# Optimization experiments

Measured on AMD Instinct MI355X. Metric: run time of the kernel, lower is better.

Reference implementation:

```python
import jax, jax.numpy as jnp
import numpy as np

CHANNELS = 512
SE_CHANNELS = 32


def setup_inputs() -> dict:
    key = jax.random.key(0)
    k_x, k_w1, k_b1, k_w2, k_b2 = jax.random.split(key, 5)
    c, se = CHANNELS, SE_CHANNELS
    x = jax.random.normal(k_x, (256, c, 32, 32), dtype=jnp.float32)
    # torch.nn.Linear default init: U(-1/sqrt(fan_in), 1/sqrt(fan_in))
    s1 = 1.0 / np.sqrt(c)
    s2 = 1.0 / np.sqrt(se)
    fc1_w = jax.random.uniform(k_w1, (se, c), jnp.float32, -s1, s1)
    fc1_b = jax.random.uniform(k_b1, (se,), jnp.float32, -s1, s1)
    fc2_w = jax.random.uniform(k_w2, (2 * c, se), jnp.float32, -s2, s2)
    fc2_b = jax.random.uniform(k_b2, (2 * c,), jnp.float32, -s2, s2)
    return {"x": x, "fc1_w": fc1_w, "fc1_b": fc1_b, "fc2_w": fc2_w, "fc2_b": fc2_b}


def reference(x, fc1_w, fc1_b, fc2_w, fc2_b):
    b, c, h, w = x.shape
    # squeeze: global average pool -> [B, C]
    y = jnp.mean(x, axis=(2, 3))
    # excitation MLP
    y = jax.nn.relu(y @ fc1_w.T + fc1_b)          # [B, se]
    y = y @ fc2_w.T + fc2_b                        # [B, 2C]
    scale, bias = y[:, :c], y[:, c:]
    scale = jax.nn.sigmoid(scale)[:, :, None, None]  # [B, C, 1, 1]
    bias = bias[:, :, None, None]
    return x * scale + bias
```

## Files before the change

kernel.cpp:

```cpp
#include <hip/hip_runtime.h>
#include <math.h>

#define BATCH 256
#define CH 512
#define SE_CH 32
#define HW 1024
#define CHUNK_B 64
#define NCHUNK (BATCH / CHUNK_B)
#define CHUNK_PLANES (CHUNK_B * CH)

typedef float f32x4 __attribute__((ext_vector_type(4)));

__global__ void se_mean_kernel(const float* __restrict__ x,
                               float* __restrict__ mean,
                               int nplanes) {
    const int lane = threadIdx.x & 63;
    const int wave_in_block = threadIdx.x >> 6;
    const int waves_per_block = blockDim.x >> 6;
    int wid = blockIdx.x * waves_per_block + wave_in_block;
    const int nwaves = gridDim.x * waves_per_block;

    for (int p = wid; p < nplanes; p += nwaves) {
        const f32x4* px = (const f32x4*)(x + (size_t)p * HW);
        float s = 0.0f;
#pragma unroll
        for (int j = 0; j < 4; ++j) {
            f32x4 v = px[lane + j * 64];
            s += (v.x + v.y) + (v.z + v.w);
        }
#pragma unroll
        for (int off = 32; off > 0; off >>= 1)
            s += __shfl_down(s, off, 64);
        if (lane == 0)
            mean[p] = s * (1.0f / (float)HW);
    }
}

__global__ void se_fc_kernel(const float* __restrict__ mean,
                             const float* __restrict__ fc1_w,
                             const float* __restrict__ fc1_b,
                             const float* __restrict__ fc2_w,
                             const float* __restrict__ fc2_b,
                             float* __restrict__ scale,
                             float* __restrict__ bias) {
    const int b = blockIdx.x;
    const int t = threadIdx.x;
    __shared__ float m[CH];
    __shared__ float se[SE_CH];

    for (int i = t; i < CH; i += blockDim.x)
        m[i] = mean[b * CH + i];
    __syncthreads();

    {
        const int o = t >> 3;
        const int p = t & 7;
        float acc = 0.0f;
        const float* wr = fc1_w + o * CH + p * 64;
        const float* mr = m + p * 64;
#pragma unroll 16
        for (int k = 0; k < 64; ++k)
            acc = fmaf(wr[k], mr[k], acc);
#pragma unroll
        for (int off = 4; off > 0; off >>= 1)
            acc += __shfl_xor(acc, off, 8);
        if (p == 0)
            se[o] = fmaxf(acc + fc1_b[o], 0.0f);
    }
    __syncthreads();

    for (int o = t; o < 2 * CH; o += blockDim.x) {
        float acc = fc2_b[o];
        const float* wr = fc2_w + o * SE_CH;
#pragma unroll
        for (int k = 0; k < SE_CH; ++k)
            acc = fmaf(wr[k], se[k], acc);
        if (o < CH)
            scale[b * CH + o] = 1.0f / (1.0f + expf(-acc));
        else
            bias[b * CH + (o - CH)] = acc;
    }
}

__global__ void se_apply_kernel(const float* __restrict__ x,
                                const float* __restrict__ scale,
                                const float* __restrict__ bias,
                                float* __restrict__ out,
                                size_t n4) {
    size_t i = blockIdx.x * (size_t)blockDim.x + threadIdx.x;
    const size_t stride = (size_t)gridDim.x * blockDim.x;
    const f32x4* x4 = (const f32x4*)x;
    f32x4* o4 = (f32x4*)out;

    for (; i < n4; i += stride) {
        const int plane = (int)(i >> 8);
        const float s = scale[plane];
        const float bi = bias[plane];
        f32x4 v = x4[i];
        f32x4 r;
        r.x = fmaf(v.x, s, bi);
        r.y = fmaf(v.y, s, bi);
        r.z = fmaf(v.z, s, bi);
        r.w = fmaf(v.w, s, bi);
        __builtin_nontemporal_store(r, &o4[i]);
    }
}

extern "C" void kernel_launch(void* const* d_in, const int* in_sizes, int n_in,
                              void* d_out, int out_size, void* d_ws, size_t ws_size,
                              hipStream_t stream) {
    const float* x     = (const float*)d_in[0];
    const float* fc1_w = (const float*)d_in[1];
    const float* fc1_b = (const float*)d_in[2];
    const float* fc2_w = (const float*)d_in[3];
    const float* fc2_b = (const float*)d_in[4];
    float* out = (float*)d_out;

    const int nplanes = BATCH * CH;
    float* mean  = (float*)d_ws;
    float* scale = mean + nplanes;
    float* bias  = scale + nplanes;

    for (int ck = 0; ck < NCHUNK; ++ck) {
        const size_t po = (size_t)ck * CHUNK_PLANES;
        const float* xc = x + po * HW;
        float* oc = out + po * HW;

        se_mean_kernel<<<1024, 256, 0, stream>>>(xc, mean + po, CHUNK_PLANES);

        se_fc_kernel<<<CHUNK_B, 256, 0, stream>>>(mean + po, fc1_w, fc1_b,
                                                  fc2_w, fc2_b,
                                                  scale + po, bias + po);

        se_apply_kernel<<<2048, 256, 0, stream>>>(xc, scale + po, bias + po, oc,
                                                  (size_t)CHUNK_PLANES * (HW / 4));
    }
}
```

Baseline: 303.6 us.

## Fuse FC into apply blocks and overlap next chunk's mean with current apply

Replaces the three kernels per chunk with one fused kernel. Apply blocks recompute the small FC MLP locally for their 64-channel slice, and extra blocks compute the channel means of the next chunk in the same launch. This software-pipelines the mean pass against the apply pass, so the mean read of chunk k+1 can hit cache while chunk k is written. It also removes the separate FC launch. In exchange, fc1 is computed redundantly 8 times per batch element, and the mean and apply blocks compete for bandwidth inside each launch.

```diff
diff --git a/kernel.cpp b/kernel.cpp
--- a/kernel.cpp
+++ b/kernel.cpp
@@ -8,101 +8,104 @@
 #define CHUNK_B 64
 #define NCHUNK (BATCH / CHUNK_B)
 #define CHUNK_PLANES (CHUNK_B * CH)
+#define SUBS 8
+#define CPS (CH / SUBS)
+#define NA_BLOCKS (CHUNK_B * SUBS)
+#define NM_BLOCKS 512
 
 typedef float f32x4 __attribute__((ext_vector_type(4)));
 
-__global__ void se_mean_kernel(const float* __restrict__ x,
-                               float* __restrict__ mean,
-                               int nplanes) {
-    const int lane = threadIdx.x & 63;
-    const int wave_in_block = threadIdx.x >> 6;
-    const int waves_per_block = blockDim.x >> 6;
-    int wid = blockIdx.x * waves_per_block + wave_in_block;
-    const int nwaves = gridDim.x * waves_per_block;
-
-    for (int p = wid; p < nplanes; p += nwaves) {
-        const f32x4* px = (const f32x4*)(x + (size_t)p * HW);
-        float s = 0.0f;
-#pragma unroll
-        for (int j = 0; j < 4; ++j) {
-            f32x4 v = px[lane + j * 64];
-            s += (v.x + v.y) + (v.z + v.w);
-        }
-#pragma unroll
-        for (int off = 32; off > 0; off >>= 1)
-            s += __shfl_down(s, off, 64);
-        if (lane == 0)
-            mean[p] = s * (1.0f / (float)HW);
-    }
-}
-
-__global__ void se_fc_kernel(const float* __restrict__ mean,
-                             const float* __restrict__ fc1_w,
-                             const float* __restrict__ fc1_b,
-                             const float* __restrict__ fc2_w,
-                             const float* __restrict__ fc2_b,
-                             float* __restrict__ scale,
-                             float* __restrict__ bias) {
-    const int b = blockIdx.x;
+__global__ __launch_bounds__(256) void se_fused(
+        const float* __restrict__ x,
+        float* __restrict__ out,
+        float* __restrict__ mean_ws,
+        const float* __restrict__ fc1_w,
+        const float* __restrict__ fc1_b,
+        const float* __restrict__ fc2_w,
+        const float* __restrict__ fc2_b,
+        int na, int apply_b0, int mean_p0, int mean_np) {
     const int t = threadIdx.x;
     __shared__ float m[CH];
     __shared__ float se[SE_CH];
+    __shared__ float sc[CPS];
+    __shared__ float bi[CPS];
 
-    for (int i = t; i < CH; i += blockDim.x)
-        m[i] = mean[b * CH + i];
-    __syncthreads();
+    if ((int)blockIdx.x < na) {
+        const int ab = blockIdx.x;
+        const int b = apply_b0 + (ab >> 3);
+        const int sub = ab & 7;
 
-    {
-        const int o = t >> 3;
-        const int p = t & 7;
-        float acc = 0.0f;
-        const float* wr = fc1_w + o * CH + p * 64;
-        const float* mr = m + p * 64;
-#pragma unroll 16
-        for (int k = 0; k < 64; ++k)
-            acc = fmaf(wr[k], mr[k], acc);
+        for (int i = t; i < CH; i += 256)
+            m[i] = mean_ws[(size_t)b * CH + i];
+        __syncthreads();
+
+        {
+            const int o = t >> 3;
+            const int p = t & 7;
+            const float* wr = fc1_w + o * CH;
+            float acc = 0.0f;
 #pragma unroll
-        for (int off = 4; off > 0; off >>= 1)
-            acc += __shfl_xor(acc, off, 8);
-        if (p == 0)
-            se[o] = fmaxf(acc + fc1_b[o], 0.0f);
-    }
-    __syncthreads();
+            for (int j = 0; j < 64; ++j) {
+                const int k = p + 8 * j;
+                acc = fmaf(wr[k], m[k], acc);
+            }
+            acc += __shfl_xor(acc, 4, 8);
+            acc += __shfl_xor(acc, 2, 8);
+            acc += __shfl_xor(acc, 1, 8);
+            if (p == 0)
+                se[o] = fmaxf(acc + fc1_b[o], 0.0f);
+        }
+        __syncthreads();
 
-    for (int o = t; o < 2 * CH; o += blockDim.x) {
-        float acc = fc2_b[o];
-        const float* wr = fc2_w + o * SE_CH;
+        if (t < 2 * CPS) {
+            const int c = sub * CPS + (t & (CPS - 1));
+            const int o = (t < CPS) ? c : (CH + c);
+            float acc = fc2_b[o];
+            const float* wr = fc2_w + o * SE_CH;
 #pragma unroll
-        for (int k = 0; k < SE_CH; ++k)
-            acc = fmaf(wr[k], se[k], acc);
-        if (o < CH)
-            scale[b * CH + o] = 1.0f / (1.0f + expf(-acc));
-        else
-            bias[b * CH + (o - CH)] = acc;
-    }
-}
+            for (int k = 0; k < SE_CH; ++k)
+                acc = fmaf(wr[k], se[k], acc);
+            if (t < CPS)
+                sc[t] = 1.0f / (1.0f + expf(-acc));
+            else
+                bi[t - CPS] = acc;
+        }
+        __syncthreads();
 
-__global__ void se_apply_kernel(const float* __restrict__ x,
-                                const float* __restrict__ scale,
-                                const float* __restrict__ bias,
-                                float* __restrict__ out,
-                                size_t n4) {
-    size_t i = blockIdx.x * (size_t)blockDim.x + threadIdx.x;
-    const size_t stride = (size_t)gridDim.x * blockDim.x;
-    const f32x4* x4 = (const f32x4*)x;
-    f32x4* o4 = (f32x4*)out;
-
-    for (; i < n4; i += stride) {
-        const int plane = (int)(i >> 8);
-        const float s = scale[plane];
-        const float bi = bias[plane];
-        f32x4 v = x4[i];
-        f32x4 r;
-        r.x = fmaf(v.x, s, bi);
-        r.y = fmaf(v.y, s, bi);
-        r.z = fmaf(v.z, s, bi);
-        r.w = fmaf(v.w, s, bi);
-        __builtin_nontemporal_store(r, &o4[i]);
+        const size_t base = ((size_t)b * CH + (size_t)sub * CPS) * HW;
+        const f32x4* xp = (const f32x4*)(x + base);
+        f32x4* op = (f32x4*)(out + base);
+#pragma unroll 4
+        for (int p = 0; p < CPS; ++p) {
+            const float s = sc[p];
+            const float bb = bi[p];
+            f32x4 v = xp[p * 256 + t];
+            f32x4 r;
+            r.x = fmaf(v.x, s, bb);
+            r.y = fmaf(v.y, s, bb);
+            r.z = fmaf(v.z, s, bb);
+            r.w = fmaf(v.w, s, bb);
+            __builtin_nontemporal_store(r, &op[p * 256 + t]);
+        }
+    } else {
+        const int lane = t & 63;
+        const int wib = t >> 6;
+        int wid = ((int)blockIdx.x - na) * 4 + wib;
+        const int nw = ((int)gridDim.x - na) * 4;
+        for (int p = wid; p < mean_np; p += nw) {
+            const f32x4* px = (const f32x4*)(x + (size_t)(mean_p0 + p) * HW);
+            float s = 0.0f;
+#pragma unroll
+            for (int j = 0; j < 4; ++j) {
+                f32x4 v = px[lane + j * 64];
+                s += (v.x + v.y) + (v.z + v.w);
+            }
+#pragma unroll
+            for (int off = 32; off > 0; off >>= 1)
+                s += __shfl_down(s, off, 64);
+            if (lane == 0)
+                mean_ws[mean_p0 + p] = s * (1.0f / (float)HW);
+        }
     }
 }
 
@@ -115,24 +118,18 @@
     const float* fc2_w = (const float*)d_in[3];
     const float* fc2_b = (const float*)d_in[4];
     float* out = (float*)d_out;
+    float* mean = (float*)d_ws;
 
-    const int nplanes = BATCH * CH;
-    float* mean  = (float*)d_ws;
-    float* scale = mean + nplanes;
-    float* bias  = scale + nplanes;
+    se_fused<<<2048, 256, 0, stream>>>(x, out, mean, fc1_w, fc1_b, fc2_w, fc2_b,
+                                       0, 0, 0, CHUNK_PLANES);
 
-    for (int ck = 0; ck < NCHUNK; ++ck) {
-        const size_t po = (size_t)ck * CHUNK_PLANES;
-        const float* xc = x + po * HW;
-        float* oc = out + po * HW;
+    for (int k = 0; k < NCHUNK - 1; ++k) {
+        se_fused<<<NA_BLOCKS + NM_BLOCKS, 256, 0, stream>>>(
+            x, out, mean, fc1_w, fc1_b, fc2_w, fc2_b,
+            NA_BLOCKS, k * CHUNK_B, (k + 1) * CHUNK_PLANES, CHUNK_PLANES);
+    }
 
-        se_mean_kernel<<<1024, 256, 0, stream>>>(xc, mean + po, CHUNK_PLANES);
-
-        se_fc_kernel<<<CHUNK_B, 256, 0, stream>>>(mean + po, fc1_w, fc1_b,
-                                                  fc2_w, fc2_b,
-                                                  scale + po, bias + po);
-
-        se_apply_kernel<<<2048, 256, 0, stream>>>(xc, scale + po, bias + po, oc,
-                                                  (size_t)CHUNK_PLANES * (HW / 4));
-    }
+    se_fused<<<NA_BLOCKS, 256, 0, stream>>>(
+        x, out, mean, fc1_w, fc1_b, fc2_w, fc2_b,
+        NA_BLOCKS, (NCHUNK - 1) * CHUNK_B, 0, 0);
 }
```

Result: faster. 279.7 us (-7.9%).
